# Optimization experiments

Measured on AMD Instinct MI355X. Metric: run time of the kernel, lower is better.

Reference implementation:

```python
import jax, jax.numpy as jnp
import numpy as np

L, H, D, E, F, T, B, V = 6, 6, 64, 384, 1536, 256, 256, 65


def setup_inputs() -> dict:
    key = jax.random.key(0)
    ks = iter(jax.random.split(key, 32))
    s = 0.02
    n = lambda shape: jax.random.normal(next(ks), shape, dtype=jnp.float32) * s
    inp = {
        "inputs": jax.random.randint(next(ks), (B, T), 0, V),
        "targets": jax.random.randint(next(ks), (B, T), 0, V),
        "tok_emb": n((V, E)),
        "pos_emb": n((T, E)),
        "Wq": n((L, H, E, D)),
        "Wk": n((L, H, E, D)),
        "Wv": n((L, H, E, D)),
        "Wo": n((L, E, E)),
        "bo": jnp.zeros((L, E), jnp.float32),
        "ln1_g": jnp.ones((L, E), jnp.float32),
        "ln1_b": jnp.zeros((L, E), jnp.float32),
        "W1": n((L, E, F)),
        "b1": jnp.zeros((L, F), jnp.float32),
        "W2": n((L, F, E)),
        "b2": jnp.zeros((L, E), jnp.float32),
        "ln2_g": jnp.ones((L, E), jnp.float32),
        "ln2_b": jnp.zeros((L, E), jnp.float32),
        "lnf_g": jnp.ones((E,), jnp.float32),
        "lnf_b": jnp.zeros((E,), jnp.float32),
        "Wh": n((E, V)),
        "bh": jnp.zeros((V,), jnp.float32),
    }
    return inp


def _layer_norm(x, g, b, eps=1e-5):
    mu = jnp.mean(x, axis=-1, keepdims=True)
    var = jnp.var(x, axis=-1, keepdims=True)
    return (x - mu) * jax.lax.rsqrt(var + eps) * g + b


def _forward(inputs, targets, tok_emb, pos_emb, Wq, Wk, Wv, Wo, bo,
             ln1_g, ln1_b, W1, b1, W2, b2, ln2_g, ln2_b, lnf_g, lnf_b, Wh, bh):
    Bc, Tc = inputs.shape
    x = tok_emb[inputs] + pos_emb[:Tc]  # [B,T,E]
    causal = jnp.tril(jnp.ones((Tc, Tc), bool))
    scale = D ** -0.5
    for l in range(L):
        h = _layer_norm(x, ln1_g[l], ln1_b[l])
        q = jnp.einsum('bte,hed->bhtd', h, Wq[l])
        k = jnp.einsum('bte,hed->bhtd', h, Wk[l])
        v = jnp.einsum('bte,hed->bhtd', h, Wv[l])
        scores = jnp.einsum('bhtd,bhsd->bhts', q, k) * scale
        scores = jnp.where(causal, scores, -jnp.inf)
        att = jax.nn.softmax(scores, axis=-1)
        o = jnp.einsum('bhts,bhsd->bhtd', att, v)
        o = o.transpose(0, 2, 1, 3).reshape(Bc, Tc, E)  # concat heads
        x = x + o @ Wo[l] + bo[l]
        h2 = _layer_norm(x, ln2_g[l], ln2_b[l])
        x = x + jax.nn.relu(h2 @ W1[l] + b1[l]) @ W2[l] + b2[l]
    x = _layer_norm(x, lnf_g, lnf_b)
    logits = x @ Wh + bh  # [B,T,V]
    logp = jax.nn.log_softmax(logits, axis=-1)
    nll = -jnp.take_along_axis(logp, targets[..., None], axis=-1)[..., 0]
    loss = jnp.mean(nll)
    return logits.reshape(Bc * Tc, V), loss


def reference(inputs, targets, tok_emb, pos_emb, Wq, Wk, Wv, Wo, bo,
              ln1_g, ln1_b, W1, b1, W2, b2, ln2_g, ln2_b, lnf_g, lnf_b, Wh, bh):
    return _forward(inputs, targets, tok_emb, pos_emb, Wq, Wk, Wv, Wo, bo,
                    ln1_g, ln1_b, W1, b1, W2, b2, ln2_g, ln2_b, lnf_g, lnf_b, Wh, bh)
```

## Files before the change

### kernel.cpp

```cpp
#include <hip/hip_runtime.h>
#include <math.h>

#define LL 6
#define HH 6
#define EE 384
#define FF 1536
#define TT 256
#define BB 256
#define VV 65
constexpr int BT = BB * TT;

typedef __attribute__((ext_vector_type(8))) short s16x8;
typedef __attribute__((ext_vector_type(4))) float f32x4;
typedef __attribute__((ext_vector_type(2))) unsigned int u32x2;
typedef unsigned int uint;
typedef unsigned short ushort_t;

__device__ __forceinline__ float uaf(uint u) { union { uint u; float f; } c; c.u = u; return c.f; }
__device__ __forceinline__ ushort_t f2b(float f) {
  union { float f; uint u; } c; c.f = f;
  uint r = c.u + 0x7fffu + ((c.u >> 16) & 1u);
  return (ushort_t)(r >> 16);
}
__device__ __forceinline__ float b2f(ushort_t b) { return uaf((uint)b << 16); }
__device__ __forceinline__ float blo(uint u) { return uaf(u << 16); }
__device__ __forceinline__ float bhi(uint u) { return uaf(u & 0xffff0000u); }
__device__ __forceinline__ uint pack2(float a, float b) {
  return (uint)f2b(a) | ((uint)f2b(b) << 16);
}

__device__ __forceinline__ void gload_lds16(const void* g, void* l) {
  __builtin_amdgcn_global_load_lds(
      (const __attribute__((address_space(1))) unsigned int*)g,
      (__attribute__((address_space(3))) unsigned int*)l, 16, 0, 0);
}

__global__ __launch_bounds__(256)
void embed_ln(const int* __restrict__ inp, const float* __restrict__ tok,
              const float* __restrict__ pos, const float* __restrict__ g,
              const float* __restrict__ b, ushort_t* __restrict__ x,
              ushort_t* __restrict__ outp) {
  int wid = threadIdx.x >> 6, lane = threadIdx.x & 63;
  int row = blockIdx.x * 4 + wid;
  int t = row % TT;
  int tk = inp[row];
  const float* tr = tok + (size_t)tk * EE;
  const float* pr = pos + (size_t)t * EE;
  float v[6];
  float s = 0.f, s2 = 0.f;
#pragma unroll
  for (int i = 0; i < 3; ++i) {
    int e = 2 * lane + 128 * i;
    float2 a = *(const float2*)&tr[e];
    float2 p2 = *(const float2*)&pr[e];
    v[2 * i] = a.x + p2.x;
    v[2 * i + 1] = a.y + p2.y;
    s += v[2 * i] + v[2 * i + 1];
    s2 += v[2 * i] * v[2 * i] + v[2 * i + 1] * v[2 * i + 1];
  }
#pragma unroll
  for (int off = 32; off; off >>= 1) {
    s += __shfl_xor(s, off);
    s2 += __shfl_xor(s2, off);
  }
  float mu = s * (1.f / EE);
  float var = s2 * (1.f / EE) - mu * mu;
  float rs = rsqrtf(var + 1e-5f);
  uint* x32 = (uint*)x;
  uint* o32 = (uint*)outp;
#pragma unroll
  for (int i = 0; i < 3; ++i) {
    int e = 2 * lane + 128 * i;
    float2 gg = *(const float2*)&g[e];
    float2 bb = *(const float2*)&b[e];
    int slot = row * 192 + lane + 64 * i;
    x32[slot] = pack2(v[2 * i], v[2 * i + 1]);
    o32[slot] = pack2((v[2 * i] - mu) * rs * gg.x + bb.x,
                      (v[2 * i + 1] - mu) * rs * gg.y + bb.y);
  }
}

__global__ __launch_bounds__(256)
void pack_qkv(const float* __restrict__ Wq, const float* __restrict__ Wk,
              const float* __restrict__ Wv, ushort_t* __restrict__ dst) {
  int idx = blockIdx.x * 256 + threadIdx.x;
  int l = idx / (1152 * 384);
  int r = idx % (1152 * 384);
  int n = r / 384;
  int k = r % 384;
  int which = n / 384;
  int hd = n % 384;
  int h = hd >> 6, d = hd & 63;
  const float* src = which == 0 ? Wq : (which == 1 ? Wk : Wv);
  dst[idx] = f2b(src[((size_t)(l * HH + h) * EE + k) * 64 + d]);
}

__global__ __launch_bounds__(256)
void pack_wt(const float* __restrict__ src, ushort_t* __restrict__ dst, int Kd, int Nd) {
  int idx = blockIdx.x * 256 + threadIdx.x;
  int l = idx / (Kd * Nd);
  int r = idx % (Kd * Nd);
  int n = r / Kd;
  int k = r % Kd;
  dst[idx] = f2b(src[((size_t)l * Kd + k) * Nd + n]);
}

__global__ __launch_bounds__(256)
void pack_head(const float* __restrict__ Wh, ushort_t* __restrict__ dst) {
  int idx = blockIdx.x * 256 + threadIdx.x;
  int n = idx / 384, k = idx % 384;
  dst[idx] = (n < VV) ? f2b(Wh[(size_t)k * VV + n]) : (ushort_t)0;
}

__global__ __launch_bounds__(256)
void ln_res_384(ushort_t* __restrict__ x, const ushort_t* __restrict__ delta,
                const float* __restrict__ g, const float* __restrict__ b,
                ushort_t* __restrict__ outp) {
  int wid = threadIdx.x >> 6, lane = threadIdx.x & 63;
  int row = blockIdx.x * 4 + wid;
  uint* x32 = (uint*)x;
  const uint* d32 = (const uint*)delta;
  float v[6];
  float s = 0.f, s2 = 0.f;
#pragma unroll
  for (int i = 0; i < 3; ++i) {
    int slot = row * 192 + lane + 64 * i;
    uint xu = x32[slot];
    uint du = d32[slot];
    v[2 * i] = blo(xu) + blo(du);
    v[2 * i + 1] = bhi(xu) + bhi(du);
    s += v[2 * i] + v[2 * i + 1];
    s2 += v[2 * i] * v[2 * i] + v[2 * i + 1] * v[2 * i + 1];
  }
#pragma unroll
  for (int off = 32; off; off >>= 1) {
    s += __shfl_xor(s, off);
    s2 += __shfl_xor(s2, off);
  }
  float mu = s * (1.f / EE);
  float var = s2 * (1.f / EE) - mu * mu;
  float rs = rsqrtf(var + 1e-5f);
  uint* o32 = (uint*)outp;
#pragma unroll
  for (int i = 0; i < 3; ++i) {
    int e = 2 * lane + 128 * i;
    float2 gg = *(const float2*)&g[e];
    float2 bb = *(const float2*)&b[e];
    int slot = row * 192 + lane + 64 * i;
    x32[slot] = pack2(v[2 * i], v[2 * i + 1]);
    o32[slot] = pack2((v[2 * i] - mu) * rs * gg.x + bb.x,
                      (v[2 * i + 1] - mu) * rs * gg.y + bb.y);
  }
}

template <int MODE, bool BIAS, bool RELU>
__global__ __launch_bounds__(256)
void gemm_bf16(const ushort_t* __restrict__ A, const ushort_t* __restrict__ Wt,
               const float* __restrict__ bias, ushort_t* __restrict__ Cb,
               float* __restrict__ Cf, ushort_t* __restrict__ Cv,
               int M, int N, int K, int nx) {
  __shared__ ushort_t sm[16896];
  ushort_t* As = sm;
  ushort_t* Bs = sm + 8192;
  const int tid = threadIdx.x;

  int bid = blockIdx.x;
  {
    const int nwg = gridDim.x;
    const int q = nwg >> 3, rr = nwg & 7;
    const int xcd = bid & 7, within = bid >> 3;
    bid = (xcd < rr ? xcd * (q + 1) : rr * (q + 1) + (xcd - rr) * q) + within;
  }
  const int bn = (bid % nx) * 128;
  const int bm = (bid / nx) * 128;

  const int w = tid >> 6, lane = tid & 63;
  const int wr = (w >> 1) * 64, wc = (w & 1) * 64;
  const int fr = lane & 15, fq = lane >> 4;

  const int rp = lane >> 2;
  const int fqs = (lane & 3) ^ ((rp >> 1) & 3);
  const ushort_t* Ag0 = A + (size_t)(bm + w * 16 + rp) * K + fqs * 8;
  const ushort_t* Ag1 = Ag0 + (size_t)64 * K;
  const ushort_t* Bg0 = Wt + (size_t)(bn + w * 16 + rp) * K + fqs * 8;
  const ushort_t* Bg1 = Bg0 + (size_t)64 * K;

  const int slotr = (fq ^ ((fr >> 1) & 3)) * 8;
  const ushort_t* Ard = As + (wr + fr) * 32 + slotr;
  const ushort_t* Brd = Bs + (wc + fr) * 32 + slotr;

  const int nt = K >> 5;
  auto STAGE = [&](int kt, int b) {
    const int k0 = kt << 5;
    const int bo = b << 12;
    gload_lds16(Ag0 + k0, As + bo + (w * 16) * 32);
    gload_lds16(Ag1 + k0, As + bo + (64 + w * 16) * 32);
    gload_lds16(Bg0 + k0, Bs + bo + (w * 16) * 32);
    gload_lds16(Bg1 + k0, Bs + bo + (64 + w * 16) * 32);
  };

  f32x4 acc[4][4] = {};
  STAGE(0, 0);

  for (int t = 0; t < nt; ++t) {
    const int bo = (t & 1) << 12;
    if (t + 1 < nt) {
      STAGE(t + 1, (t & 1) ^ 1);
      asm volatile("s_waitcnt vmcnt(4)" ::: "memory");
    } else {
      asm volatile("s_waitcnt vmcnt(0)" ::: "memory");
    }
    __builtin_amdgcn_s_barrier();
    __builtin_amdgcn_sched_barrier(0);
    s16x8 afr[4], bfr[4];
#pragma unroll
    for (int m = 0; m < 4; ++m) afr[m] = *(const s16x8*)(Ard + bo + m * 512);
#pragma unroll
    for (int n = 0; n < 4; ++n) bfr[n] = *(const s16x8*)(Brd + bo + n * 512);
#pragma unroll
    for (int m = 0; m < 4; ++m)
#pragma unroll
      for (int n = 0; n < 4; ++n)
        acc[m][n] = __builtin_amdgcn_mfma_f32_16x16x32_bf16(afr[m], bfr[n], acc[m][n], 0, 0, 0);
    __builtin_amdgcn_sched_barrier(0);
    __builtin_amdgcn_s_barrier();
  }

  if constexpr (MODE == 0 || MODE == 3) {
    if (MODE == 3 && bn >= 768) {
      const int r0 = bm + wr + fq * 4;
      const int c0 = bn + wc + fr;
#pragma unroll
      for (int n = 0; n < 4; ++n) {
        const int col = c0 + n * 16 - 768;
#pragma unroll
        for (int m = 0; m < 4; ++m) {
          const int row = r0 + m * 16;
          uint lo = (uint)f2b(acc[m][n][0]) | ((uint)f2b(acc[m][n][1]) << 16);
          uint hi = (uint)f2b(acc[m][n][2]) | ((uint)f2b(acc[m][n][3]) << 16);
          *(u32x2*)&Cv[(size_t)col * M + row] = u32x2{lo, hi};
        }
      }
      return;
    }
    const int ostride = (MODE == 3) ? 768 : N;
#pragma unroll
    for (int n = 0; n < 4; ++n) {
      const int col = wc + n * 16 + fr;
      const float bv = BIAS ? bias[bn + col] : 0.f;
#pragma unroll
      for (int m = 0; m < 4; ++m) {
        const int row = wr + m * 16 + fq * 4;
#pragma unroll
        for (int j = 0; j < 4; ++j) {
          float vv = acc[m][n][j] + bv;
          if constexpr (RELU) vv = fmaxf(vv, 0.f);
          sm[(row + j) * 132 + col] = f2b(vv);
        }
      }
    }
    __syncthreads();
    const int rr2 = tid >> 4, cb = (tid & 15) * 8;
#pragma unroll
    for (int pp = 0; pp < 8; ++pp) {
      const int row = pp * 16 + rr2;
      s16x8 v8 = *(const s16x8*)(sm + row * 132 + cb);
      *(s16x8*)(Cb + (size_t)(bm + row) * ostride + bn + cb) = v8;
    }
    return;
  }
  const int r0 = bm + wr + fq * 4;
  const int c0 = bn + wc + fr;
#pragma unroll
  for (int n = 0; n < 4; ++n) {
    const int col = c0 + n * 16;
    if (col >= VV) continue;
    const float bv = BIAS ? bias[col] : 0.f;
#pragma unroll
    for (int m = 0; m < 4; ++m) {
      const int row = r0 + m * 16;
#pragma unroll
      for (int j = 0; j < 4; ++j)
        Cf[(size_t)(row + j) * VV + col] = acc[m][n][j] + bv;
    }
  }
}

__global__ __launch_bounds__(512, 4)
void attn_kernel(const ushort_t* __restrict__ qk, const ushort_t* __restrict__ vt,
                 ushort_t* __restrict__ o, int R) {
  __shared__ ushort_t Ks[16384];
  __shared__ ushort_t Vs[16512];
  __shared__ ushort_t Pb[8][640];
  const int tid = threadIdx.x;
  const int w = tid >> 6, lane = tid & 63;
  const int seq = blockIdx.x / HH, hh = blockIdx.x % HH;
  const int brow = seq * TT;

  {
    const ushort_t* kbase = qk + (size_t)brow * 768 + 384 + hh * 64;
#pragma unroll
    for (int cc = 0; cc < 4; ++cc) {
      const int ci = cc * 512 + tid;
      const int s = ci >> 3, j = ci & 7;
      const int srcb = (j * 16) ^ ((s & 7) << 4);
      gload_lds16(kbase + (size_t)s * 768 + (srcb >> 1), Ks + cc * 4096 + w * 512);
    }
  }
  {
    s16x8 vreg[4];
    int vidx[4];
#pragma unroll
    for (int t2 = 0; t2 < 4; ++t2) {
      const int ci = t2 * 512 + tid;
      const int d = ci >> 5, c2 = ci & 31;
      vidx[t2] = d * 258 + c2 * 8;
      vreg[t2] = *(const s16x8*)(vt + (size_t)(hh * 64 + d) * R + brow + c2 * 8);
    }
#pragma unroll
    for (int t2 = 0; t2 < 4; ++t2)
      *(s16x8*)(Vs + vidx[t2]) = vreg[t2];
  }
  __syncthreads();

  const int r = lane & 15, g = lane >> 4;
  ushort_t* pw = &Pb[w][0];

#pragma unroll
  for (int qti = 0; qti < 2; ++qti) {
    const int qt = qti ? (15 - w) : w;
    const int q0 = qt << 4;
    const int n_st = qt + 1;
    const ushort_t* qrow = qk + (size_t)(brow + q0 + r) * 768 + hh * 64 + g * 8;
    const s16x8 qa0 = *(const s16x8*)qrow;
    const s16x8 qa1 = *(const s16x8*)(qrow + 32);

    f32x4 S[16];
#pragma unroll
    for (int st = 0; st < 16; ++st) {
      if (st < n_st) {
        const int srow = st * 16 + r;
        const int sw = (srow & 7) << 4;
        const s16x8 kb0 = *(const s16x8*)(Ks + ((srow * 128 + ((g * 16) ^ sw)) >> 1));
        const s16x8 kb1 = *(const s16x8*)(Ks + ((srow * 128 + ((64 + g * 16) ^ sw)) >> 1));
        f32x4 t = {0.f, 0.f, 0.f, 0.f};
        t = __builtin_amdgcn_mfma_f32_16x16x32_bf16(qa0, kb0, t, 0, 0, 0);
        t = __builtin_amdgcn_mfma_f32_16x16x32_bf16(qa1, kb1, t, 0, 0, 0);
        if (st == n_st - 1) {
#pragma unroll
          for (int j = 0; j < 4; ++j)
            t[j] = (r <= g * 4 + j) ? t[j] : -1e30f;
        }
        S[st] = t;
      }
    }

    float mrow[4] = {-1e30f, -1e30f, -1e30f, -1e30f};
#pragma unroll
    for (int st = 0; st < 16; ++st)
      if (st < n_st) {
#pragma unroll
        for (int j = 0; j < 4; ++j) mrow[j] = fmaxf(mrow[j], S[st][j]);
      }
#pragma unroll
    for (int j = 0; j < 4; ++j) {
      float m = mrow[j];
      m = fmaxf(m, __shfl_xor(m, 1));
      m = fmaxf(m, __shfl_xor(m, 2));
      m = fmaxf(m, __shfl_xor(m, 4));
      m = fmaxf(m, __shfl_xor(m, 8));
      mrow[j] = m;
    }

    float rsum[4] = {0.f, 0.f, 0.f, 0.f};
    f32x4 O[4] = {f32x4{0,0,0,0}, f32x4{0,0,0,0}, f32x4{0,0,0,0}, f32x4{0,0,0,0}};
    const int n_sc = (n_st + 1) >> 1;
#pragma unroll
    for (int sc = 0; sc < 8; ++sc) {
      if (sc < n_sc) {
#pragma unroll
        for (int tt = 0; tt < 2; ++tt) {
          const int st = sc * 2 + tt;
#pragma unroll
          for (int j = 0; j < 4; ++j) {
            float p = 0.f;
            if (st < n_st) p = __expf((S[st][j] - mrow[j]) * 0.125f);
            rsum[j] += p;
            pw[(g * 4 + j) * 40 + tt * 16 + r] = f2b(p);
          }
        }
        const s16x8 pa = *(const s16x8*)(pw + r * 40 + g * 8);
#pragma unroll
        for (int dt = 0; dt < 4; ++dt) {
          const s16x8 vb = *(const s16x8*)(Vs + (dt * 16 + r) * 258 + sc * 32 + g * 8);
          O[dt] = __builtin_amdgcn_mfma_f32_16x16x32_bf16(pa, vb, O[dt], 0, 0, 0);
        }
      }
    }

#pragma unroll
    for (int j = 0; j < 4; ++j) {
      float s = rsum[j];
      s += __shfl_xor(s, 1);
      s += __shfl_xor(s, 2);
      s += __shfl_xor(s, 4);
      s += __shfl_xor(s, 8);
      rsum[j] = 1.f / s;
    }
    ushort_t* obase = o + (size_t)(brow + q0 + g * 4) * 384 + hh * 64 + r;
#pragma unroll
    for (int j = 0; j < 4; ++j)
#pragma unroll
      for (int dt = 0; dt < 4; ++dt)
        obase[(size_t)j * 384 + dt * 16] = f2b(O[dt][j] * rsum[j]);
  }
}

__global__ __launch_bounds__(256)
void loss_kernel(const float* __restrict__ logits, const int* __restrict__ targets,
                 float* __restrict__ loss_acc, int R) {
  __shared__ float red[4];
  int wid = threadIdx.x >> 6, lane = threadIdx.x & 63;
  float lsum = 0.f;
  for (int r = blockIdx.x * 4 + wid; r < R; r += gridDim.x * 4) {
    const float* lrow = logits + (size_t)r * VV;
    float v = lrow[lane];
    float e64 = lrow[64];
    float m = fmaxf(v, e64);
#pragma unroll
    for (int off = 32; off; off >>= 1) m = fmaxf(m, __shfl_xor(m, off));
    float s = expf(v - m);
#pragma unroll
    for (int off = 32; off; off >>= 1) s += __shfl_xor(s, off);
    s += expf(e64 - m);
    float lse = m + logf(s);
    int t = targets[r];
    float tv = (t < 64) ? __shfl(v, t) : e64;
    lsum += lse - tv;
  }
  if (lane == 0) red[wid] = lsum;
  __syncthreads();
  if (threadIdx.x == 0)
    atomicAdd(loss_acc, (red[0] + red[1] + red[2] + red[3]) * (1.f / BT));
}

extern "C" void kernel_launch(void* const* d_in, const int* in_sizes, int n_in,
                              void* d_out, int out_size, void* d_ws, size_t ws_size,
                              hipStream_t stream) {
  const int* inputs = (const int*)d_in[0];
  const int* targets = (const int*)d_in[1];
  const float* tok_emb = (const float*)d_in[2];
  const float* pos_emb = (const float*)d_in[3];
  const float* Wq = (const float*)d_in[4];
  const float* Wk = (const float*)d_in[5];
  const float* Wv = (const float*)d_in[6];
  const float* Wo = (const float*)d_in[7];
  const float* bo = (const float*)d_in[8];
  const float* ln1_g = (const float*)d_in[9];
  const float* ln1_b = (const float*)d_in[10];
  const float* W1 = (const float*)d_in[11];
  const float* b1 = (const float*)d_in[12];
  const float* W2 = (const float*)d_in[13];
  const float* b2 = (const float*)d_in[14];
  const float* ln2_g = (const float*)d_in[15];
  const float* ln2_b = (const float*)d_in[16];
  const float* lnf_g = (const float*)d_in[17];
  const float* lnf_b = (const float*)d_in[18];
  const float* Wh = (const float*)d_in[19];
  const float* bh = (const float*)d_in[20];

  float* logits = (float*)d_out;
  float* loss = logits + (size_t)BT * VV;

  auto al = [](size_t b) { return (b + 255) & ~(size_t)255; };
  const size_t wq_b = al((size_t)LL * 1152 * 384 * 2);
  const size_t wo_b = al((size_t)LL * 384 * 384 * 2);
  const size_t w1_b = al((size_t)LL * 1536 * 384 * 2);
  const size_t wh_b = al((size_t)128 * 384 * 2);
  const size_t wfix = wq_b + wo_b + 2 * w1_b + wh_b;

  int c = BB;
  while (c > 1 && wfix + (size_t)c * 256 * 6144 > ws_size) c >>= 1;
  const int R = c * TT;
  const int nch = BB / c;

  char* p = (char*)d_ws;
  ushort_t* wqkv = (ushort_t*)p; p += wq_b;
  ushort_t* wot  = (ushort_t*)p; p += wo_b;
  ushort_t* w1t  = (ushort_t*)p; p += w1_b;
  ushort_t* w2t  = (ushort_t*)p; p += w1_b;
  ushort_t* whb  = (ushort_t*)p; p += wh_b;
  ushort_t* x = (ushort_t*)p;    p += (size_t)R * 768;
  ushort_t* hb = (ushort_t*)p;   p += (size_t)R * 768;
  ushort_t* ob = (ushort_t*)p;   p += (size_t)R * 768;
  ushort_t* un = (ushort_t*)p;
  ushort_t* qkb = un;
  ushort_t* vtb = un + (size_t)R * 768;
  ushort_t* midb = un;

  hipMemsetAsync(loss, 0, 4, stream);
  pack_qkv<<<LL * 1152 * 384 / 256, 256, 0, stream>>>(Wq, Wk, Wv, wqkv);
  pack_wt<<<LL * 384 * 384 / 256, 256, 0, stream>>>(Wo, wot, 384, 384);
  pack_wt<<<LL * 384 * 1536 / 256, 256, 0, stream>>>(W1, w1t, 384, 1536);
  pack_wt<<<LL * 1536 * 384 / 256, 256, 0, stream>>>(W2, w2t, 1536, 384);
  pack_head<<<128 * 384 / 256, 256, 0, stream>>>(Wh, whb);

  const int my = R / 128;
  for (int ch = 0; ch < nch; ++ch) {
    const size_t r0 = (size_t)ch * R;
    embed_ln<<<R / 4, 256, 0, stream>>>(inputs + r0, tok_emb, pos_emb,
                                        ln1_g, ln1_b, x, hb);
    for (int l = 0; l < LL; ++l) {
      gemm_bf16<3, false, false><<<9 * my, 256, 0, stream>>>(
          hb, wqkv + (size_t)l * 1152 * 384, nullptr, qkb, nullptr, vtb, R, 1152, 384, 9);
      attn_kernel<<<c * HH, 512, 0, stream>>>(qkb, vtb, ob, R);
      gemm_bf16<0, true, false><<<3 * my, 256, 0, stream>>>(
          ob, wot + (size_t)l * 384 * 384, bo + l * EE, hb, nullptr, nullptr, R, 384, 384, 3);
      ln_res_384<<<R / 4, 256, 0, stream>>>(x, hb, ln2_g + l * EE, ln2_b + l * EE, hb);
      gemm_bf16<0, true, true><<<12 * my, 256, 0, stream>>>(
          hb, w1t + (size_t)l * 1536 * 384, b1 + l * FF, midb, nullptr, nullptr, R, 1536, 384, 12);
      gemm_bf16<0, true, false><<<3 * my, 256, 0, stream>>>(
          midb, w2t + (size_t)l * 384 * 1536, b2 + l * EE, hb, nullptr, nullptr, R, 384, 1536, 3);
      if (l + 1 < LL)
        ln_res_384<<<R / 4, 256, 0, stream>>>(x, hb, ln1_g + (l + 1) * EE,
                                              ln1_b + (l + 1) * EE, hb);
      else
        ln_res_384<<<R / 4, 256, 0, stream>>>(x, hb, lnf_g, lnf_b, hb);
    }
    gemm_bf16<2, true, false><<<1 * my, 256, 0, stream>>>(
        hb, whb, bh, nullptr, logits + r0 * VV, nullptr, R, 128, 384, 1);
    loss_kernel<<<1024, 256, 0, stream>>>(logits + r0 * VV, targets + r0, loss, R);
  }
}
```

Baseline: 2.911 ms.

## Fuse output-projection GEMMs with residual add and LayerNorm in one kernel

```diff
diff --git a/kernel.cpp b/kernel.cpp
--- a/kernel.cpp
+++ b/kernel.cpp
@@ -112,47 +112,6 @@
   dst[idx] = (n < VV) ? f2b(Wh[(size_t)k * VV + n]) : (ushort_t)0;
 }
 
-__global__ __launch_bounds__(256)
-void ln_res_384(ushort_t* __restrict__ x, const ushort_t* __restrict__ delta,
-                const float* __restrict__ g, const float* __restrict__ b,
-                ushort_t* __restrict__ outp) {
-  int wid = threadIdx.x >> 6, lane = threadIdx.x & 63;
-  int row = blockIdx.x * 4 + wid;
-  uint* x32 = (uint*)x;
-  const uint* d32 = (const uint*)delta;
-  float v[6];
-  float s = 0.f, s2 = 0.f;
-#pragma unroll
-  for (int i = 0; i < 3; ++i) {
-    int slot = row * 192 + lane + 64 * i;
-    uint xu = x32[slot];
-    uint du = d32[slot];
-    v[2 * i] = blo(xu) + blo(du);
-    v[2 * i + 1] = bhi(xu) + bhi(du);
-    s += v[2 * i] + v[2 * i + 1];
-    s2 += v[2 * i] * v[2 * i] + v[2 * i + 1] * v[2 * i + 1];
-  }
-#pragma unroll
-  for (int off = 32; off; off >>= 1) {
-    s += __shfl_xor(s, off);
-    s2 += __shfl_xor(s2, off);
-  }
-  float mu = s * (1.f / EE);
-  float var = s2 * (1.f / EE) - mu * mu;
-  float rs = rsqrtf(var + 1e-5f);
-  uint* o32 = (uint*)outp;
-#pragma unroll
-  for (int i = 0; i < 3; ++i) {
-    int e = 2 * lane + 128 * i;
-    float2 gg = *(const float2*)&g[e];
-    float2 bb = *(const float2*)&b[e];
-    int slot = row * 192 + lane + 64 * i;
-    x32[slot] = pack2(v[2 * i], v[2 * i + 1]);
-    o32[slot] = pack2((v[2 * i] - mu) * rs * gg.x + bb.x,
-                      (v[2 * i + 1] - mu) * rs * gg.y + bb.y);
-  }
-}
-
 template <int MODE, bool BIAS, bool RELU>
 __global__ __launch_bounds__(256)
 void gemm_bf16(const ushort_t* __restrict__ A, const ushort_t* __restrict__ Wt,
@@ -283,6 +242,128 @@
       for (int j = 0; j < 4; ++j)
         Cf[(size_t)(row + j) * VV + col] = acc[m][n][j] + bv;
     }
+  }
+}
+
+__global__ __launch_bounds__(512, 4)
+void gemm_resln(const ushort_t* __restrict__ A, const ushort_t* __restrict__ Wt,
+                const float* __restrict__ bias, ushort_t* __restrict__ x,
+                const float* __restrict__ g, const float* __restrict__ b,
+                ushort_t* __restrict__ outp, int M, int K) {
+  __shared__ ushort_t sm[32768];
+  ushort_t* As = sm;
+  ushort_t* Bs = sm + 8192;
+  const int tid = threadIdx.x;
+  const int bm = blockIdx.x * 128;
+  const int w = tid >> 6, lane = tid & 63;
+  const int wm = w >> 2, wn = w & 3;
+  const int wr = wm * 64, wc = wn * 96;
+  const int fr = lane & 15, fq = lane >> 4;
+
+  const int rp = lane >> 2;
+  const int fqs = (lane & 3) ^ ((rp >> 1) & 3);
+  const ushort_t* Ag = A + (size_t)(bm + w * 16 + rp) * K + fqs * 8;
+  const ushort_t* Bg = Wt + (size_t)(w * 16 + rp) * K + fqs * 8;
+
+  const int slotr = (fq ^ ((fr >> 1) & 3)) * 8;
+  const ushort_t* Ard = As + (wr + fr) * 32 + slotr;
+  const ushort_t* Brd = Bs + (wc + fr) * 32 + slotr;
+
+  const int nt = K >> 5;
+  auto STAGE = [&](int kt, int bsel) {
+    const int k0 = kt << 5;
+    gload_lds16(Ag + k0, As + (bsel ? 4096 : 0) + (w * 16) * 32);
+    const int bo = bsel ? 12288 : 0;
+#pragma unroll
+    for (int gi = 0; gi < 3; ++gi)
+      gload_lds16(Bg + (size_t)(128 * gi) * K + k0,
+                  Bs + bo + (gi * 128 + w * 16) * 32);
+  };
+
+  f32x4 acc[4][6] = {};
+  STAGE(0, 0);
+
+  for (int t = 0; t < nt; ++t) {
+    const int aob = (t & 1) ? 4096 : 0;
+    const int bob = (t & 1) ? 12288 : 0;
+    if (t + 1 < nt) {
+      STAGE(t + 1, (t & 1) ^ 1);
+      asm volatile("s_waitcnt vmcnt(4)" ::: "memory");
+    } else {
+      asm volatile("s_waitcnt vmcnt(0)" ::: "memory");
+    }
+    __builtin_amdgcn_s_barrier();
+    __builtin_amdgcn_sched_barrier(0);
+    s16x8 afr[4], bfr[6];
+#pragma unroll
+    for (int m = 0; m < 4; ++m) afr[m] = *(const s16x8*)(Ard + aob + m * 512);
+#pragma unroll
+    for (int n = 0; n < 6; ++n) bfr[n] = *(const s16x8*)(Brd + bob + n * 512);
+#pragma unroll
+    for (int m = 0; m < 4; ++m)
+#pragma unroll
+      for (int n = 0; n < 6; ++n)
+        acc[m][n] = __builtin_amdgcn_mfma_f32_16x16x32_bf16(afr[m], bfr[n], acc[m][n], 0, 0, 0);
+    __builtin_amdgcn_sched_barrier(0);
+    __builtin_amdgcn_s_barrier();
+  }
+
+  uint* x32 = (uint*)x;
+  uint* o32 = (uint*)outp;
+  const uint* smu = (const uint*)sm;
+#pragma unroll
+  for (int h = 0; h < 2; ++h) {
+    if (wm == h) {
+#pragma unroll
+      for (int n = 0; n < 6; ++n) {
+        const int col = wc + n * 16 + fr;
+        const float bv = bias[col];
+#pragma unroll
+        for (int m = 0; m < 4; ++m) {
+          const int rr = m * 16 + fq * 4;
+#pragma unroll
+          for (int j = 0; j < 4; ++j)
+            sm[(rr + j) * 388 + col] = f2b(acc[m][n][j] + bv);
+        }
+      }
+    }
+    __syncthreads();
+#pragma unroll
+    for (int rr = 0; rr < 8; ++rr) {
+      const int rih = w * 8 + rr;
+      const int row = h * 64 + rih;
+      const int du = rih * 194 + lane * 3;
+      uint d0 = smu[du + 0], d1 = smu[du + 1], d2 = smu[du + 2];
+      const size_t xs = (size_t)(bm + row) * 192 + lane * 3;
+      uint xu0 = x32[xs + 0], xu1 = x32[xs + 1], xu2 = x32[xs + 2];
+      float v0 = blo(d0) + blo(xu0), v1 = bhi(d0) + bhi(xu0);
+      float v2 = blo(d1) + blo(xu1), v3 = bhi(d1) + bhi(xu1);
+      float v4 = blo(d2) + blo(xu2), v5 = bhi(d2) + bhi(xu2);
+      float s = v0 + v1 + v2 + v3 + v4 + v5;
+      float s2 = v0 * v0 + v1 * v1 + v2 * v2 + v3 * v3 + v4 * v4 + v5 * v5;
+#pragma unroll
+      for (int off = 32; off; off >>= 1) {
+        s += __shfl_xor(s, off);
+        s2 += __shfl_xor(s2, off);
+      }
+      float mu = s * (1.f / EE);
+      float var = s2 * (1.f / EE) - mu * mu;
+      float rs = rsqrtf(var + 1e-5f);
+      const int e = lane * 6;
+      float2 g01 = *(const float2*)&g[e + 0];
+      float2 g23 = *(const float2*)&g[e + 2];
+      float2 g45 = *(const float2*)&g[e + 4];
+      float2 b01 = *(const float2*)&b[e + 0];
+      float2 b23 = *(const float2*)&b[e + 2];
+      float2 b45 = *(const float2*)&b[e + 4];
+      x32[xs + 0] = pack2(v0, v1);
+      x32[xs + 1] = pack2(v2, v3);
+      x32[xs + 2] = pack2(v4, v5);
+      o32[xs + 0] = pack2((v0 - mu) * rs * g01.x + b01.x, (v1 - mu) * rs * g01.y + b01.y);
+      o32[xs + 1] = pack2((v2 - mu) * rs * g23.x + b23.x, (v3 - mu) * rs * g23.y + b23.y);
+      o32[xs + 2] = pack2((v4 - mu) * rs * g45.x + b45.x, (v5 - mu) * rs * g45.y + b45.y);
+    }
+    __syncthreads();
   }
 }
 
@@ -514,18 +595,15 @@
       gemm_bf16<3, false, false><<<9 * my, 256, 0, stream>>>(
           hb, wqkv + (size_t)l * 1152 * 384, nullptr, qkb, nullptr, vtb, R, 1152, 384, 9);
       attn_kernel<<<c * HH, 512, 0, stream>>>(qkb, vtb, ob, R);
-      gemm_bf16<0, true, false><<<3 * my, 256, 0, stream>>>(
-          ob, wot + (size_t)l * 384 * 384, bo + l * EE, hb, nullptr, nullptr, R, 384, 384, 3);
-      ln_res_384<<<R / 4, 256, 0, stream>>>(x, hb, ln2_g + l * EE, ln2_b + l * EE, hb);
+      gemm_resln<<<my, 512, 0, stream>>>(
+          ob, wot + (size_t)l * 384 * 384, bo + l * EE, x,
+          ln2_g + l * EE, ln2_b + l * EE, hb, R, 384);
       gemm_bf16<0, true, true><<<12 * my, 256, 0, stream>>>(
           hb, w1t + (size_t)l * 1536 * 384, b1 + l * FF, midb, nullptr, nullptr, R, 1536, 384, 12);
-      gemm_bf16<0, true, false><<<3 * my, 256, 0, stream>>>(
-          midb, w2t + (size_t)l * 384 * 1536, b2 + l * EE, hb, nullptr, nullptr, R, 384, 1536, 3);
-      if (l + 1 < LL)
-        ln_res_384<<<R / 4, 256, 0, stream>>>(x, hb, ln1_g + (l + 1) * EE,
-                                              ln1_b + (l + 1) * EE, hb);
-      else
-        ln_res_384<<<R / 4, 256, 0, stream>>>(x, hb, lnf_g, lnf_b, hb);
+      const float* ng = (l + 1 < LL) ? ln1_g + (l + 1) * EE : lnf_g;
+      const float* nb = (l + 1 < LL) ? ln1_b + (l + 1) * EE : lnf_b;
+      gemm_resln<<<my, 512, 0, stream>>>(
+          midb, w2t + (size_t)l * 384 * 1536, b2 + l * EE, x, ng, nb, hb, R, 1536);
     }
     gemm_bf16<2, true, false><<<1 * my, 256, 0, stream>>>(
         hb, whb, bh, nullptr, logits + r0 * VV, nullptr, R, 128, 384, 1);
```

After: 4.158 ms. 1.43x slower.
